# Kernel optimization log

Hardware: AMD Instinct MI355X
Metric: run time of the kernel (lower is better)

## Reference

```python
import jax, jax.numpy as jnp
import numpy as np

N = 50000       # nodes
E = 1600000     # edges (avg degree 32)
IN = 64         # in_channels
ED = 16         # edge_dim
H = 128         # hidden_channels


def setup_inputs() -> dict:
    key = jax.random.key(0)
    ks = jax.random.split(key, 32)
    rn = lambda k, shape, s: jax.random.normal(k, shape, jnp.float32) * s
    inp = {}
    inp['x'] = rn(ks[0], (N, IN), 1.0)
    inp['edge_index'] = jax.random.randint(ks[1], (2, E), 0, N, dtype=jnp.int64)
    inp['edge_attr'] = rn(ks[2], (E, ED), 1.0)
    # per-layer params: edge linear (ED -> node_dim), MLP (d_in->H, H->H)
    node_dims = [IN, H, H]
    i = 3
    for l, d in enumerate(node_dims):
        inp[f'We{l}'] = rn(ks[i], (ED, d), 1.0 / np.sqrt(ED)); i += 1
        inp[f'be{l}'] = jnp.zeros((d,), jnp.float32)
        inp[f'W1_{l}'] = rn(ks[i], (d, H), 1.0 / np.sqrt(d)); i += 1
        inp[f'b1_{l}'] = jnp.zeros((H,), jnp.float32)
        inp[f'W2_{l}'] = rn(ks[i], (H, H), 1.0 / np.sqrt(H)); i += 1
        inp[f'b2_{l}'] = jnp.zeros((H,), jnp.float32)
    inp['Wlin'] = rn(ks[i], (H, 1), 1.0 / np.sqrt(H))
    inp['blin'] = jnp.zeros((1,), jnp.float32)
    return inp


def gine_conv(x, src, dst, ea, We, be, W1, b1, W2, b2):
    # message: relu(x_j + Lin_e(edge_attr)); aggregate: sum into dst; eps=0
    msg = jax.nn.relu(x[src] + ea @ We + be)            # [E, d]
    agg = jax.ops.segment_sum(msg, dst, num_segments=x.shape[0])  # [N, d]
    h = x + agg                                          # (1+eps)*x + agg, eps=0
    return jax.nn.relu(h @ W1 + b1) @ W2 + b2            # MLP


def reference(x, edge_index, edge_attr,
              We0, be0, W1_0, b1_0, W2_0, b2_0,
              We1, be1, W1_1, b1_1, W2_1, b2_1,
              We2, be2, W1_2, b1_2, W2_2, b2_2,
              Wlin, blin):
    src, dst = edge_index[0], edge_index[1]
    h = jax.nn.relu(gine_conv(x, src, dst, edge_attr, We0, be0, W1_0, b1_0, W2_0, b2_0))
    h = jax.nn.relu(gine_conv(h, src, dst, edge_attr, We1, be1, W1_1, b1_1, W2_1, b2_1))
    h = jax.nn.relu(gine_conv(h, src, dst, edge_attr, We2, be2, W1_2, b1_2, W2_2, b2_2))
    out = jax.nn.sigmoid(h @ Wlin + blin)                # [N, 1]
    return out.squeeze(-1)                               # [N]
```

## Files before the change

### kernel.cpp

```cpp
#include <hip/hip_runtime.h>
#include <math.h>


#define BLK 256

typedef __attribute__((ext_vector_type(2))) float f32x2;

__device__ inline f32x2 pk_fma(f32x2 a, f32x2 b, f32x2 c) {
    f32x2 d;
    asm("v_pk_fma_f32 %0, %1, %2, %3" : "=v"(d) : "v"(a), "v"(b), "v"(c));
    return d;
}


__global__ void detect_kernel(const unsigned int* __restrict__ ei, int* __restrict__ flag) {
    int t = blockIdx.x * blockDim.x + threadIdx.x;
    if (t < 1024) {
        if (ei[2 * t + 1] != 0u) atomicOr(flag, 1);
    }
}

__global__ void convert_hist_kernel(const int* __restrict__ ei32, const long long* __restrict__ ei64,
                                    const int* __restrict__ flag, int E,
                                    int* __restrict__ src, unsigned int* __restrict__ drank,
                                    int* __restrict__ counts) {
    int e = blockIdx.x * blockDim.x + threadIdx.x;
    if (e >= E) return;
    int s, d;
    if (*flag) { s = ei32[e]; d = ei32[E + e]; }
    else       { s = (int)ei64[e]; d = (int)ei64[E + e]; }
    src[e] = s;
    unsigned int r = (unsigned int)atomicAdd(&counts[d], 1);
    drank[e] = (unsigned int)d | (r << 16);
}

__global__ void scan_kernel(const int* __restrict__ counts, int* __restrict__ offsets, int n) {
    __shared__ int tsum[256];
    __shared__ int texcl[256];
    int t = threadIdx.x;
    int chunk = (n + 255) >> 8;
    int b = t * chunk, e = min(b + chunk, n);
    int s = 0;
    for (int i = b; i < e; i++) s += counts[i];
    tsum[t] = s;
    __syncthreads();
    if (t == 0) {
        int run = 0;
        for (int i = 0; i < 256; i++) { texcl[i] = run; run += tsum[i]; }
        offsets[n] = run;
    }
    __syncthreads();
    int run = texcl[t];
    for (int i = b; i < e; i++) { offsets[i] = run; run += counts[i]; }
}

__global__ void scatter_perm_kernel(const unsigned int* __restrict__ drank,
                                    const int* __restrict__ offsets,
                                    int* __restrict__ perm, int E) {
    int e = blockIdx.x * blockDim.x + threadIdx.x;
    if (e >= E) return;
    unsigned int v = drank[e];
    perm[offsets[v & 0xffffu] + (int)(v >> 16)] = e;
}

__global__ __launch_bounds__(256) void gather_ea_kernel(
    const int* __restrict__ perm, const int* __restrict__ src32,
    const float4* __restrict__ ea4,
    int* __restrict__ srcp, float4* __restrict__ eap4, int E) {
    int t = blockIdx.x * blockDim.x + threadIdx.x;
    int p = t >> 2, q = t & 3;
    if (p >= E) return;
    int e = perm[p];
    if (q == 0) srcp[p] = src32[e];
    eap4[(size_t)p * 4 + q] = ea4[(size_t)e * 4 + q];
}

template <int D>
__global__ __launch_bounds__(256) void aggregate_kernel(
    const float* __restrict__ x, const float* __restrict__ eap,
    const int* __restrict__ srcp,
    const float* __restrict__ We, const float* __restrict__ be,
    const int* __restrict__ offsets,
    float* __restrict__ h, int n) {
    constexpr int C = D / 64;
    int lane = threadIdx.x & 63;
    int node = __builtin_amdgcn_readfirstlane(blockIdx.x * 4 + (threadIdx.x >> 6));
    if (node >= n) return;
    int c0 = lane * C;

    f32x2 wp[C][8];
#pragma unroll
    for (int j = 0; j < C; j++)
#pragma unroll
        for (int t = 0; t < 8; t++) {
            f32x2 v; v.x = We[(2 * t) * D + c0 + j]; v.y = We[(2 * t + 1) * D + c0 + j];
            wp[j][t] = v;
        }
    float bias[C], acc[C];
#pragma unroll
    for (int j = 0; j < C; j++) {
        bias[j] = be[c0 + j];
        acc[j] = x[(size_t)node * D + c0 + j];
    }
    int p = offsets[node], pe = offsets[node + 1];

    for (; p + 4 <= pe; p += 4) {
        int s0 = srcp[p], s1 = srcp[p + 1], s2 = srcp[p + 2], s3 = srcp[p + 3];
        float xv[4][C];
        {
            const float* r0 = x + (size_t)s0 * D + c0;
            const float* r1 = x + (size_t)s1 * D + c0;
            const float* r2 = x + (size_t)s2 * D + c0;
            const float* r3 = x + (size_t)s3 * D + c0;
            if constexpr (C == 2) {
                float2 t0 = *(const float2*)r0, t1 = *(const float2*)r1;
                float2 t2 = *(const float2*)r2, t3 = *(const float2*)r3;
                xv[0][0] = t0.x; xv[0][1] = t0.y; xv[1][0] = t1.x; xv[1][1] = t1.y;
                xv[2][0] = t2.x; xv[2][1] = t2.y; xv[3][0] = t3.x; xv[3][1] = t3.y;
            } else {
                xv[0][0] = *r0; xv[1][0] = *r1; xv[2][0] = *r2; xv[3][0] = *r3;
            }
        }
#pragma unroll
        for (int u = 0; u < 4; u++) {
            const float4* er = (const float4*)(eap + (size_t)(p + u) * 16);
            float4 e0 = er[0], e1 = er[1], e2 = er[2], e3 = er[3];
            f32x2 ev[8];
            ev[0].x = e0.x; ev[0].y = e0.y;  ev[1].x = e0.z; ev[1].y = e0.w;
            ev[2].x = e1.x; ev[2].y = e1.y;  ev[3].x = e1.z; ev[3].y = e1.w;
            ev[4].x = e2.x; ev[4].y = e2.y;  ev[5].x = e2.z; ev[5].y = e2.w;
            ev[6].x = e3.x; ev[6].y = e3.y;  ev[7].x = e3.z; ev[7].y = e3.w;
#pragma unroll
            for (int j = 0; j < C; j++) {
                f32x2 prod; prod.x = xv[u][j] + bias[j]; prod.y = 0.f;
#pragma unroll
                for (int t = 0; t < 8; t++) prod = pk_fma(ev[t], wp[j][t], prod);
                acc[j] += fmaxf(prod.x + prod.y, 0.f);
            }
        }
    }
    for (; p < pe; p++) {
        int s = srcp[p];
        const float* xr = x + (size_t)s * D + c0;
        float xv[C];
        if constexpr (C == 2) { float2 t = *(const float2*)xr; xv[0] = t.x; xv[1] = t.y; }
        else xv[0] = *xr;
        const float4* er = (const float4*)(eap + (size_t)p * 16);
        float4 e0 = er[0], e1 = er[1], e2 = er[2], e3 = er[3];
        f32x2 ev[8];
        ev[0].x = e0.x; ev[0].y = e0.y;  ev[1].x = e0.z; ev[1].y = e0.w;
        ev[2].x = e1.x; ev[2].y = e1.y;  ev[3].x = e1.z; ev[3].y = e1.w;
        ev[4].x = e2.x; ev[4].y = e2.y;  ev[5].x = e2.z; ev[5].y = e2.w;
        ev[6].x = e3.x; ev[6].y = e3.y;  ev[7].x = e3.z; ev[7].y = e3.w;
#pragma unroll
        for (int j = 0; j < C; j++) {
            f32x2 prod; prod.x = xv[j] + bias[j]; prod.y = 0.f;
#pragma unroll
            for (int t = 0; t < 8; t++) prod = pk_fma(ev[t], wp[j][t], prod);
            acc[j] += fmaxf(prod.x + prod.y, 0.f);
        }
    }
#pragma unroll
    for (int j = 0; j < C; j++) h[(size_t)node * D + c0 + j] = acc[j];
}

template <int K>
__global__ __launch_bounds__(256) void gemm_kernel(
    const float* __restrict__ A, const float* __restrict__ B,
    const float* __restrict__ bias, float* __restrict__ C, int n) {
    __shared__ __align__(16) float As[16][68];
    __shared__ __align__(16) float Bs[16][128];
    int t = threadIdx.x;
    int row0 = blockIdx.x * 64;
    int tr = t >> 5, tc = t & 31;
    float acc[8][4];
#pragma unroll
    for (int r = 0; r < 8; r++)
#pragma unroll
        for (int c = 0; c < 4; c++) acc[r][c] = 0.f;

    int lr = t >> 2, lk = (t & 3) * 4;
    int bk = t >> 4, bc = (t & 15) * 8;

    int grow = row0 + lr;
    const float* aptr = A + (size_t)grow * K + lk;
    float4 a;
    if (grow < n) a = *(const float4*)aptr;
    else a = make_float4(0.f, 0.f, 0.f, 0.f);
    const float4* bp = (const float4*)(B + (size_t)bk * 128 + bc);
    float4 b0 = bp[0], b1 = bp[1];

#pragma unroll 1
    for (int ks = 0; ks < K; ks += 16) {
        As[lk + 0][lr] = a.x; As[lk + 1][lr] = a.y;
        As[lk + 2][lr] = a.z; As[lk + 3][lr] = a.w;
        *(float4*)&Bs[bk][bc] = b0;
        *(float4*)&Bs[bk][bc + 4] = b1;
        __syncthreads();
        if (ks + 16 < K) {
            if (grow < n) a = *(const float4*)(aptr + ks + 16);
            const float4* bp2 = (const float4*)(B + (size_t)(ks + 16 + bk) * 128 + bc);
            b0 = bp2[0]; b1 = bp2[1];
        }
#pragma unroll
        for (int kk = 0; kk < 16; kk++) {
            float4 a0 = *(const float4*)&As[kk][tr * 8];
            float4 a1 = *(const float4*)&As[kk][tr * 8 + 4];
            float4 bv = *(const float4*)&Bs[kk][tc * 4];
            float ar[8] = {a0.x, a0.y, a0.z, a0.w, a1.x, a1.y, a1.z, a1.w};
            float bc4[4] = {bv.x, bv.y, bv.z, bv.w};
#pragma unroll
            for (int r = 0; r < 8; r++)
#pragma unroll
                for (int c = 0; c < 4; c++) acc[r][c] = fmaf(ar[r], bc4[c], acc[r][c]);
        }
        __syncthreads();
    }
    float4 bb = *(const float4*)(bias + tc * 4);
#pragma unroll
    for (int r = 0; r < 8; r++) {
        int gr = row0 + tr * 8 + r;
        if (gr < n) {
            float4 v;
            v.x = fmaxf(acc[r][0] + bb.x, 0.f);
            v.y = fmaxf(acc[r][1] + bb.y, 0.f);
            v.z = fmaxf(acc[r][2] + bb.z, 0.f);
            v.w = fmaxf(acc[r][3] + bb.w, 0.f);
            *(float4*)(C + (size_t)gr * 128 + tc * 4) = v;
        }
    }
}

__global__ __launch_bounds__(256) void final_kernel(
    const float* __restrict__ x, const float* __restrict__ Wlin,
    const float* __restrict__ blin, float* __restrict__ out, int n) {
    int lane = threadIdx.x & 63;
    int node = blockIdx.x * 4 + (threadIdx.x >> 6);
    if (node >= n) return;
    float2 w = *(const float2*)(Wlin + lane * 2);
    float2 xv = *(const float2*)(x + (size_t)node * 128 + lane * 2);
    float v = xv.x * w.x + xv.y * w.y;
#pragma unroll
    for (int off = 32; off; off >>= 1) v += __shfl_down(v, off, 64);
    if (lane == 0) out[node] = 1.f / (1.f + expf(-(v + blin[0])));
}

extern "C" void kernel_launch(void* const* d_in, const int* in_sizes, int n_in,
                              void* d_out, int out_size, void* d_ws, size_t ws_size,
                              hipStream_t stream) {
    const float* x_in = (const float*)d_in[0];
    const void* ei    = d_in[1];
    const float* ea   = (const float*)d_in[2];
    const float* We[3]  = {(const float*)d_in[3], (const float*)d_in[9],  (const float*)d_in[15]};
    const float* be[3]  = {(const float*)d_in[4], (const float*)d_in[10], (const float*)d_in[16]};
    const float* W1[3]  = {(const float*)d_in[5], (const float*)d_in[11], (const float*)d_in[17]};
    const float* b1[3]  = {(const float*)d_in[6], (const float*)d_in[12], (const float*)d_in[18]};
    const float* W2[3]  = {(const float*)d_in[7], (const float*)d_in[13], (const float*)d_in[19]};
    const float* b2[3]  = {(const float*)d_in[8], (const float*)d_in[14], (const float*)d_in[20]};
    const float* Wlin = (const float*)d_in[21];
    const float* blin = (const float*)d_in[22];
    float* out = (float*)d_out;

    const int N = in_sizes[0] / 64;
    const int E = in_sizes[1] / 2;

    size_t off = 0;
    auto alloc = [&](size_t bytes) {
        void* p = (char*)d_ws + off;
        off += (bytes + 255) & ~(size_t)255;
        return p;
    };
    int*          flag    = (int*)alloc(4);
    int*          src32   = (int*)alloc((size_t)E * 4);
    unsigned int* drank   = (unsigned int*)alloc((size_t)E * 4);
    int*          counts  = (int*)alloc((size_t)N * 4);
    int*          offsets = (int*)alloc((size_t)(N + 1) * 4);
    int*          perm    = (int*)alloc((size_t)E * 4);
    int*          srcp    = (int*)alloc((size_t)E * 4);
    float*        eap     = (float*)alloc((size_t)E * 16 * 4);
    float*        bufA    = (float*)alloc((size_t)N * 128 * 4);
    float*        bufB    = (float*)alloc((size_t)N * 128 * 4);
    float*        bufC    = (float*)alloc((size_t)N * 128 * 4);

    hipMemsetAsync(flag, 0, 4, stream);
    hipMemsetAsync(counts, 0, (size_t)N * 4, stream);

    int egrid = (E + BLK - 1) / BLK;
    detect_kernel<<<4, BLK, 0, stream>>>((const unsigned int*)ei, flag);
    convert_hist_kernel<<<egrid, BLK, 0, stream>>>((const int*)ei, (const long long*)ei, flag, E,
                                                   src32, drank, counts);
    scan_kernel<<<1, BLK, 0, stream>>>(counts, offsets, N);
    scatter_perm_kernel<<<egrid, BLK, 0, stream>>>(drank, offsets, perm, E);
    int g4grid = ((E * 4) + BLK - 1) / BLK;
    gather_ea_kernel<<<g4grid, BLK, 0, stream>>>(perm, src32, (const float4*)ea,
                                                 srcp, (float4*)eap, E);

    int ngrid4 = (N + 3) / 4;
    int ggrid  = (N + 63) / 64;

    aggregate_kernel<64><<<ngrid4, BLK, 0, stream>>>(x_in, eap, srcp, We[0], be[0], offsets, bufA, N);
    gemm_kernel<64><<<ggrid, BLK, 0, stream>>>(bufA, W1[0], b1[0], bufB, N);
    gemm_kernel<128><<<ggrid, BLK, 0, stream>>>(bufB, W2[0], b2[0], bufC, N);
    aggregate_kernel<128><<<ngrid4, BLK, 0, stream>>>(bufC, eap, srcp, We[1], be[1], offsets, bufA, N);
    gemm_kernel<128><<<ggrid, BLK, 0, stream>>>(bufA, W1[1], b1[1], bufB, N);
    gemm_kernel<128><<<ggrid, BLK, 0, stream>>>(bufB, W2[1], b2[1], bufC, N);
    aggregate_kernel<128><<<ngrid4, BLK, 0, stream>>>(bufC, eap, srcp, We[2], be[2], offsets, bufA, N);
    gemm_kernel<128><<<ggrid, BLK, 0, stream>>>(bufA, W1[2], b1[2], bufB, N);
    gemm_kernel<128><<<ggrid, BLK, 0, stream>>>(bufB, W2[2], b2[2], bufC, N);

    final_kernel<<<ngrid4, BLK, 0, stream>>>(bufC, Wlin, blin, out, N);
}
```

Baseline: 943.4 us.

## Fuse the two MLP GEMMs per layer into one kernel via shared memory

Replaces the two separate GEMM launches of each GINE layer's MLP with one kernel. The ReLU'd hidden tile from the first GEMM is kept transposed in shared memory and fed straight into the second GEMM. This removes the global write and read of the N×128 intermediate buffer and one launch per layer. In exchange, shared memory per block grows substantially, which can lower occupancy.

New measurement: 963.4 us. 2.1% more time.

```diff
diff --git a/kernel.cpp b/kernel.cpp
--- a/kernel.cpp
+++ b/kernel.cpp
@@ -164,12 +164,15 @@
     for (int j = 0; j < C; j++) h[(size_t)node * D + c0 + j] = acc[j];
 }
 
-template <int K>
-__global__ __launch_bounds__(256) void gemm_kernel(
-    const float* __restrict__ A, const float* __restrict__ B,
-    const float* __restrict__ bias, float* __restrict__ C, int n) {
+template <int K1>
+__global__ __launch_bounds__(256) void mlp_fused_kernel(
+    const float* __restrict__ A,
+    const float* __restrict__ W1, const float* __restrict__ b1,
+    const float* __restrict__ W2, const float* __restrict__ b2,
+    float* __restrict__ C, int n) {
     __shared__ __align__(16) float As[16][68];
     __shared__ __align__(16) float Bs[16][128];
+    __shared__ __align__(16) float C1t[128][68];
     int t = threadIdx.x;
     int row0 = blockIdx.x * 64;
     int tr = t >> 5, tc = t & 31;
@@ -183,24 +186,24 @@
     int bk = t >> 4, bc = (t & 15) * 8;
 
     int grow = row0 + lr;
-    const float* aptr = A + (size_t)grow * K + lk;
+    const float* aptr = A + (size_t)grow * K1 + lk;
     float4 a;
     if (grow < n) a = *(const float4*)aptr;
     else a = make_float4(0.f, 0.f, 0.f, 0.f);
-    const float4* bp = (const float4*)(B + (size_t)bk * 128 + bc);
-    float4 b0 = bp[0], b1 = bp[1];
+    const float4* bp = (const float4*)(W1 + (size_t)bk * 128 + bc);
+    float4 b0 = bp[0], b1v = bp[1];
 
 #pragma unroll 1
-    for (int ks = 0; ks < K; ks += 16) {
+    for (int ks = 0; ks < K1; ks += 16) {
         As[lk + 0][lr] = a.x; As[lk + 1][lr] = a.y;
         As[lk + 2][lr] = a.z; As[lk + 3][lr] = a.w;
         *(float4*)&Bs[bk][bc] = b0;
-        *(float4*)&Bs[bk][bc + 4] = b1;
+        *(float4*)&Bs[bk][bc + 4] = b1v;
         __syncthreads();
-        if (ks + 16 < K) {
+        if (ks + 16 < K1) {
             if (grow < n) a = *(const float4*)(aptr + ks + 16);
-            const float4* bp2 = (const float4*)(B + (size_t)(ks + 16 + bk) * 128 + bc);
-            b0 = bp2[0]; b1 = bp2[1];
+            const float4* bp2 = (const float4*)(W1 + (size_t)(ks + 16 + bk) * 128 + bc);
+            b0 = bp2[0]; b1v = bp2[1];
         }
 #pragma unroll
         for (int kk = 0; kk < 16; kk++) {
@@ -216,7 +219,53 @@
         }
         __syncthreads();
     }
-    float4 bb = *(const float4*)(bias + tc * 4);
+
+    {
+        float4 bb = *(const float4*)(b1 + tc * 4);
+        float bc4[4] = {bb.x, bb.y, bb.z, bb.w};
+#pragma unroll
+        for (int r = 0; r < 8; r++) {
+            int row = tr * 8 + r;
+#pragma unroll
+            for (int c = 0; c < 4; c++)
+                C1t[tc * 4 + c][row] = fmaxf(acc[r][c] + bc4[c], 0.f);
+        }
+    }
+
+#pragma unroll
+    for (int r = 0; r < 8; r++)
+#pragma unroll
+        for (int c = 0; c < 4; c++) acc[r][c] = 0.f;
+
+    {
+        const float4* wp = (const float4*)(W2 + (size_t)bk * 128 + bc);
+        b0 = wp[0]; b1v = wp[1];
+    }
+#pragma unroll 1
+    for (int ks = 0; ks < 128; ks += 16) {
+        __syncthreads();
+        *(float4*)&Bs[bk][bc] = b0;
+        *(float4*)&Bs[bk][bc + 4] = b1v;
+        __syncthreads();
+        if (ks + 16 < 128) {
+            const float4* wp2 = (const float4*)(W2 + (size_t)(ks + 16 + bk) * 128 + bc);
+            b0 = wp2[0]; b1v = wp2[1];
+        }
+#pragma unroll
+        for (int kk = 0; kk < 16; kk++) {
+            float4 a0 = *(const float4*)&C1t[ks + kk][tr * 8];
+            float4 a1 = *(const float4*)&C1t[ks + kk][tr * 8 + 4];
+            float4 bv = *(const float4*)&Bs[kk][tc * 4];
+            float ar[8] = {a0.x, a0.y, a0.z, a0.w, a1.x, a1.y, a1.z, a1.w};
+            float bc4[4] = {bv.x, bv.y, bv.z, bv.w};
+#pragma unroll
+            for (int r = 0; r < 8; r++)
+#pragma unroll
+                for (int c = 0; c < 4; c++) acc[r][c] = fmaf(ar[r], bc4[c], acc[r][c]);
+        }
+    }
+
+    float4 bb = *(const float4*)(b2 + tc * 4);
 #pragma unroll
     for (int r = 0; r < 8; r++) {
         int gr = row0 + tr * 8 + r;
@@ -279,7 +328,6 @@
     int*          srcp    = (int*)alloc((size_t)E * 4);
     float*        eap     = (float*)alloc((size_t)E * 16 * 4);
     float*        bufA    = (float*)alloc((size_t)N * 128 * 4);
-    float*        bufB    = (float*)alloc((size_t)N * 128 * 4);
     float*        bufC    = (float*)alloc((size_t)N * 128 * 4);
 
     hipMemsetAsync(flag, 0, 4, stream);
@@ -299,14 +347,11 @@
     int ggrid  = (N + 63) / 64;
 
     aggregate_kernel<64><<<ngrid4, BLK, 0, stream>>>(x_in, eap, srcp, We[0], be[0], offsets, bufA, N);
-    gemm_kernel<64><<<ggrid, BLK, 0, stream>>>(bufA, W1[0], b1[0], bufB, N);
-    gemm_kernel<128><<<ggrid, BLK, 0, stream>>>(bufB, W2[0], b2[0], bufC, N);
+    mlp_fused_kernel<64><<<ggrid, BLK, 0, stream>>>(bufA, W1[0], b1[0], W2[0], b2[0], bufC, N);
     aggregate_kernel<128><<<ngrid4, BLK, 0, stream>>>(bufC, eap, srcp, We[1], be[1], offsets, bufA, N);
-    gemm_kernel<128><<<ggrid, BLK, 0, stream>>>(bufA, W1[1], b1[1], bufB, N);
-    gemm_kernel<128><<<ggrid, BLK, 0, stream>>>(bufB, W2[1], b2[1], bufC, N);
+    mlp_fused_kernel<128><<<ggrid, BLK, 0, stream>>>(bufA, W1[1], b1[1], W2[1], b2[1], bufC, N);
     aggregate_kernel<128><<<ngrid4, BLK, 0, stream>>>(bufC, eap, srcp, We[2], be[2], offsets, bufA, N);
-    gemm_kernel<128><<<ggrid, BLK, 0, stream>>>(bufA, W1[2], b1[2], bufB, N);
-    gemm_kernel<128><<<ggrid, BLK, 0, stream>>>(bufB, W2[2], b2[2], bufC, N);
+    mlp_fused_kernel<128><<<ggrid, BLK, 0, stream>>>(bufA, W1[2], b1[2], W2[2], b2[2], bufC, N);
 
     final_kernel<<<ngrid4, BLK, 0, stream>>>(bufC, Wlin, blin, out, N);
 }
```
